# Optimization experiments

Hardware: AMD Instinct MI355X
Metric: run time of the kernel (lower is better)

## Reference

```python
import jax, jax.numpy as jnp
import numpy as np

BETA = 1.0
LENGTH = 64                      # lattice side
LATTICE_SIZE = LENGTH * LENGTH   # 4096
SAMPLE_SIZE = 16384
TWO_PI = 2.0 * np.pi


def _make_shift(length: int) -> np.ndarray:
    """Nearest-neighbour shift indices (2, L*L): roll by one site in each
    positive direction on a periodic 2D lattice, matching geometry.get_shift()."""
    idx = np.arange(length * length).reshape(length, length)
    up = np.roll(idx, -1, axis=0).reshape(-1)
    right = np.roll(idx, -1, axis=1).reshape(-1)
    return np.stack([up, right], axis=0).astype(np.int64)


def setup_inputs() -> dict:
    key = jax.random.key(0)
    k_state, = jax.random.split(key, 1)
    state = jax.random.uniform(k_state, (SAMPLE_SIZE, LATTICE_SIZE),
                               dtype=jnp.float32, minval=0.0, maxval=TWO_PI)
    shift = jnp.asarray(_make_shift(LENGTH))  # (2, lattice_size) int64 indices
    return {"state": state, "shift": shift}


def reference(state, shift):
    # state: (S, N) polar angles; shift: (n_shifts, N) neighbour indices.
    # neighbours: (S, n_shifts, N) gather along lattice dim
    neighbours = state[:, shift]
    # hamiltonian = -beta * sum cos(theta_neigh - theta); forward returns -H
    log_density = BETA * jnp.sum(
        jnp.cos(neighbours - state[:, None, :]), axis=(1, 2)
    )[:, None]  # (S, 1), matches keepdim=True
    return log_density
```

## Files before the change

### kernel.cpp

```cpp
#include <hip/hip_runtime.h>


#define LAT_L    64
#define NSITE    4096
#define BLOCK    256
#define NSAMPLE  16384
#define SPB      16
#define NBLK     (NSAMPLE / SPB)

__device__ __forceinline__ float vert_sum(const float4 a, const float4 b) {
    return __cosf(b.x - a.x) + __cosf(b.y - a.y) +
           __cosf(b.z - a.z) + __cosf(b.w - a.w);
}

__device__ __forceinline__ float horiz_sum(const float4 v, const int nbr) {
    const float n0 = __shfl(v.x, nbr, 64);
    return __cosf(v.y - v.x) + __cosf(v.z - v.y) +
           __cosf(v.w - v.z) + __cosf(n0 - v.w);
}

__global__ __launch_bounds__(BLOCK)
void xy_logdensity_kernel(const float* __restrict__ state, float* __restrict__ out) {
    const int t = threadIdx.x;
    const int l = t & 63;
    const int w = t >> 6;
    const int g = l >> 4;
    const int q = l & 15;

    const long sample = (long)blockIdx.x * SPB + w * 4 + g;
    const float4* __restrict__ row = (const float4*)(state + sample * NSITE) + q;
    const int nbr = (l & 48) | ((l + 1) & 15);

    float4 first = row[0];
    float4 cur   = first;
    float4 nxt   = row[16];

    float sum = horiz_sum(cur, nbr);

#pragma unroll 4
    for (int y = 1; y < LAT_L - 1; ++y) {
        const float4 pf = row[(y + 1) * 16];
        sum += vert_sum(cur, nxt);
        sum += horiz_sum(nxt, nbr);
        cur = nxt;
        nxt = pf;
    }
    sum += vert_sum(cur, nxt);
    sum += horiz_sum(nxt, nbr);
    sum += vert_sum(nxt, first);

#pragma unroll
    for (int off = 8; off > 0; off >>= 1)
        sum += __shfl_xor(sum, off, 16);

    if (q == 0)
        out[sample] = sum;
}

extern "C" void kernel_launch(void* const* d_in, const int* in_sizes, int n_in,
                              void* d_out, int out_size, void* d_ws, size_t ws_size,
                              hipStream_t stream) {
    const float* state = (const float*)d_in[0];
    float* out = (float*)d_out;

    xy_logdensity_kernel<<<NBLK, BLOCK, 0, stream>>>(state, out);
}
```

Before: 359.0 us.

## Split each sample's rows across two lane groups and halve samples per block

Each sample is now processed by two 16-lane groups, each covering 32 rows, with one extra halo row load to close the vertical wrap. Samples per block drop from 16 to 8, doubling the grid, and launch bounds request higher occupancy. The aim is to shorten the serial per-thread load chain and raise memory-level parallelism. The cost is a slightly larger reduction and a redundant halo read.

```diff
diff --git a/kernel.cpp b/kernel.cpp
--- a/kernel.cpp
+++ b/kernel.cpp
@@ -5,7 +5,7 @@
 #define NSITE    4096
 #define BLOCK    256
 #define NSAMPLE  16384
-#define SPB      16
+#define SPB      8
 #define NBLK     (NSAMPLE / SPB)
 
 __device__ __forceinline__ float vert_sum(const float4 a, const float4 b) {
@@ -19,42 +19,45 @@
            __cosf(v.w - v.z) + __cosf(n0 - v.w);
 }
 
-__global__ __launch_bounds__(BLOCK)
+__global__ __launch_bounds__(BLOCK, 8)
 void xy_logdensity_kernel(const float* __restrict__ state, float* __restrict__ out) {
-    const int t = threadIdx.x;
-    const int l = t & 63;
-    const int w = t >> 6;
-    const int g = l >> 4;
-    const int q = l & 15;
+    const int t    = threadIdx.x;
+    const int l    = t & 63;
+    const int w    = t >> 6;
+    const int half = l >> 5;
+    const int grp  = (l >> 4) & 1;
+    const int q    = l & 15;
 
-    const long sample = (long)blockIdx.x * SPB + w * 4 + g;
-    const float4* __restrict__ row = (const float4*)(state + sample * NSITE) + q;
+    const long sample = (long)blockIdx.x * SPB + w * 2 + half;
+    const float4* __restrict__ row = (const float4*)(state + sample * NSITE);
+    const int y0 = grp << 5;
+    const float4* __restrict__ rp = row + y0 * 16 + q;
+
     const int nbr = (l & 48) | ((l + 1) & 15);
 
-    float4 first = row[0];
-    float4 cur   = first;
-    float4 nxt   = row[16];
-
-    float sum = horiz_sum(cur, nbr);
+    float4 cur = rp[0];
+    float4 nxt = rp[16];
+    float s = horiz_sum(cur, nbr);
 
 #pragma unroll 4
-    for (int y = 1; y < LAT_L - 1; ++y) {
-        const float4 pf = row[(y + 1) * 16];
-        sum += vert_sum(cur, nxt);
-        sum += horiz_sum(nxt, nbr);
+    for (int r = 1; r < 31; ++r) {
+        const float4 pf = rp[(r + 1) * 16];
+        s += vert_sum(cur, nxt);
+        s += horiz_sum(nxt, nbr);
         cur = nxt;
         nxt = pf;
     }
-    sum += vert_sum(cur, nxt);
-    sum += horiz_sum(nxt, nbr);
-    sum += vert_sum(nxt, first);
+    s += vert_sum(cur, nxt);
+    s += horiz_sum(nxt, nbr);
+    const float4 halo = row[(y0 ^ 32) * 16 + q];
+    s += vert_sum(nxt, halo);
 
 #pragma unroll
-    for (int off = 8; off > 0; off >>= 1)
-        sum += __shfl_xor(sum, off, 16);
+    for (int off = 16; off > 0; off >>= 1)
+        s += __shfl_xor(s, off, 32);
 
-    if (q == 0)
-        out[sample] = sum;
+    if ((l & 31) == 0)
+        out[sample] = s;
 }
 
 extern "C" void kernel_launch(void* const* d_in, const int* in_sizes, int n_in,
```

Result: no change. 352.5 us (-1.8%).
